# Kernel tuning notes

Measured on AMD Instinct MI355X. Metric: run time of the kernel, lower is better.

The kernel has to match this reference:

```python
import jax, jax.numpy as jnp
import numpy as np

D_MODEL = 1024
N_HEAD = 16
HEAD_DIM = D_MODEL // N_HEAD
ROPE_BASE = 10000.0


def _weight_quant(w):
    # BitNet b1.58 ternary weight quant with per-tensor absmean scale (STE).
    scale = jnp.clip(jnp.mean(jnp.abs(w)), 1e-5, None)
    wq = jnp.clip(jnp.round(w / scale), -1.0, 1.0) * scale
    return w + jax.lax.stop_gradient(wq - w)


def _act_quant(x):
    # Per-token int8 absmax activation quant (STE).
    scale = 127.0 / jnp.clip(jnp.max(jnp.abs(x), axis=-1, keepdims=True), 1e-5, None)
    xq = jnp.clip(jnp.round(x * scale), -128.0, 127.0) / scale
    return x + jax.lax.stop_gradient(xq - x)


def _bitlinear(x, w):
    # y = act_quant(x) @ weight_quant(w).T   (torch Linear convention, no bias)
    return _act_quant(x) @ _weight_quant(w).T


def _rope(x, pos):
    # x: [B, H, T, D]; half-split rotation.
    d = x.shape[-1]
    inv_freq = 1.0 / (ROPE_BASE ** (jnp.arange(0, d, 2, dtype=jnp.float32) / d))
    ang = pos[:, None].astype(jnp.float32) * inv_freq[None, :]  # [T, D/2]
    cos, sin = jnp.cos(ang), jnp.sin(ang)
    x1, x2 = x[..., : d // 2], x[..., d // 2 :]
    return jnp.concatenate([x1 * cos - x2 * sin, x1 * sin + x2 * cos], axis=-1)


def setup_inputs() -> dict:
    key = jax.random.key(0)
    k0, k1, k2, k3, k4 = jax.random.split(key, 5)
    B, T = 2, 2048
    s = 1.0 / np.sqrt(D_MODEL)
    return {
        "x": jax.random.normal(k0, (B, T, D_MODEL), dtype=jnp.float32),
        "Wq": jax.random.normal(k1, (D_MODEL, D_MODEL), dtype=jnp.float32) * s,
        "Wk": jax.random.normal(k2, (D_MODEL, D_MODEL), dtype=jnp.float32) * s,
        "Wv": jax.random.normal(k3, (D_MODEL, D_MODEL), dtype=jnp.float32) * s,
        "Wo": jax.random.normal(k4, (D_MODEL, D_MODEL), dtype=jnp.float32) * s,
    }


def reference(x, Wq, Wk, Wv, Wo):
    B, T, C = x.shape
    pos = jnp.arange(T)
    def heads(y):
        return y.reshape(B, T, N_HEAD, HEAD_DIM).transpose(0, 2, 1, 3)  # [B,H,T,D]
    q = _rope(heads(_bitlinear(x, Wq)), pos)
    k = _rope(heads(_bitlinear(x, Wk)), pos)
    v = heads(_bitlinear(x, Wv))
    scores = jnp.einsum("bhqd,bhkd->bhqk", q, k) / jnp.sqrt(jnp.float32(HEAD_DIM))
    causal = jnp.tril(jnp.ones((T, T), dtype=bool))
    scores = jnp.where(causal[None, None], scores, jnp.finfo(scores.dtype).min)
    att = jax.nn.softmax(scores, axis=-1)
    y = jnp.einsum("bhqk,bhkd->bhqd", att, v)  # [B,H,T,D]
    y = y.transpose(0, 2, 1, 3).reshape(B, T, C)
    return _bitlinear(y, Wo)
```

## Files before the change

### kernel.cpp

```cpp
#include <hip/hip_runtime.h>
#include <hip/hip_bf16.h>
#include <math.h>

typedef __bf16 bf16_t;
typedef signed char i8_t;
typedef __attribute__((ext_vector_type(8))) __bf16 bf16x8;
typedef __attribute__((ext_vector_type(4))) __bf16 bf16x4;
typedef __attribute__((ext_vector_type(4))) float f32x4;
typedef __attribute__((ext_vector_type(4))) int i32x4;

typedef __attribute__((address_space(3))) void lds_void_t;
typedef const __attribute__((address_space(1))) void glb_void_t;
#define GLOAD_LDS(g, l) __builtin_amdgcn_global_load_lds((glb_void_t*)(g), (lds_void_t*)(l), 16, 0, 0)

#define MFMA16(a,b,c) __builtin_amdgcn_mfma_f32_16x16x32_bf16(a,b,c,0,0,0)
#define MFMAI8(a,b,c) __builtin_amdgcn_mfma_i32_16x16x64_i8(a,b,c,0,0,0)

#if __has_builtin(__builtin_amdgcn_exp2f)
#define EXP2F(x) __builtin_amdgcn_exp2f(x)
#else
#define EXP2F(x) exp2f(x)
#endif

static constexpr int TSEQ = 2048;
static constexpr int CDIM = 1024;
#define NEG_BIG (-1.0e30f)
#define Q_PRESCALE 0.18033688011112042f
#define ROPE_C 0.41524101190971284f

__global__ __launch_bounds__(256) void wreduce(const float* __restrict__ W0, const float* __restrict__ W1,
                                               const float* __restrict__ W2, const float* __restrict__ W3,
                                               double* __restrict__ partial) {
  int w = blockIdx.x >> 6, b = blockIdx.x & 63;
  const float* W = (w==0)?W0:(w==1)?W1:(w==2)?W2:W3;
  const float* base = W + (size_t)b * 16384;
  double s = 0.0;
  for (int i = threadIdx.x * 4; i < 16384; i += 1024) {
    float4 v = *(const float4*)(base + i);
    s += (double)fabsf(v.x) + (double)fabsf(v.y) + (double)fabsf(v.z) + (double)fabsf(v.w);
  }
  #pragma unroll
  for (int off = 1; off < 64; off <<= 1) s += __shfl_xor(s, off);
  __shared__ double red[4];
  if ((threadIdx.x & 63) == 0) red[threadIdx.x >> 6] = s;
  __syncthreads();
  if (threadIdx.x == 0) partial[blockIdx.x] = red[0] + red[1] + red[2] + red[3];
}

__global__ __launch_bounds__(256) void prep(const float* __restrict__ W0, const float* __restrict__ W1,
                                            const float* __restrict__ W2, const float* __restrict__ W3,
                                            const double* __restrict__ partial, float* __restrict__ wscale,
                                            i8_t* __restrict__ wq_all,
                                            const float* __restrict__ xg, i8_t* __restrict__ xqg,
                                            float* __restrict__ rowfac, float2* __restrict__ ropetab) {
  int bid = blockIdx.x;
  if (bid < 4096) {
    int w = bid >> 10;
    double ssum = 0.0;
    for (int i = 0; i < 64; ++i) ssum += partial[w * 64 + i];
    float s = fmaxf((float)(ssum * (1.0 / 1048576.0)), 1e-5f);
    if ((bid & 1023) == 0 && threadIdx.x == 0) wscale[w] = s;
    const float* W = (w==0)?W0:(w==1)?W1:(w==2)?W2:W3;
    int off = ((bid & 1023) * 256 + threadIdx.x) * 4;
    float4 v = *(const float4*)(W + off);
    char4 q;
    q.x = (i8_t)(int)fminf(fmaxf(rintf(v.x / s), -1.f), 1.f);
    q.y = (i8_t)(int)fminf(fmaxf(rintf(v.y / s), -1.f), 1.f);
    q.z = (i8_t)(int)fminf(fmaxf(rintf(v.z / s), -1.f), 1.f);
    q.w = (i8_t)(int)fminf(fmaxf(rintf(v.w / s), -1.f), 1.f);
    *(char4*)(wq_all + (size_t)w * 1048576 + off) = q;
  } else if (bid < 8192) {
    int r = bid - 4096;
    float4 v = *(const float4*)(xg + (size_t)r * 1024 + threadIdx.x * 4);
    float mx = fmaxf(fmaxf(fabsf(v.x), fabsf(v.y)), fmaxf(fabsf(v.z), fabsf(v.w)));
    #pragma unroll
    for (int off = 1; off < 64; off <<= 1) mx = fmaxf(mx, __shfl_xor(mx, off));
    __shared__ float red[4];
    if ((threadIdx.x & 63) == 0) red[threadIdx.x >> 6] = mx;
    __syncthreads();
    mx = fmaxf(fmaxf(red[0], red[1]), fmaxf(red[2], red[3]));
    mx = fmaxf(mx, 1e-5f);
    float scale = 127.0f / mx;
    if (threadIdx.x == 0) rowfac[r] = mx * (1.0f / 127.0f);
    char4 q;
    q.x = (i8_t)(int)fminf(fmaxf(rintf(v.x * scale), -128.f), 127.f);
    q.y = (i8_t)(int)fminf(fmaxf(rintf(v.y * scale), -128.f), 127.f);
    q.z = (i8_t)(int)fminf(fmaxf(rintf(v.z * scale), -128.f), 127.f);
    q.w = (i8_t)(int)fminf(fmaxf(rintf(v.w * scale), -128.f), 127.f);
    *(char4*)(xqg + (size_t)r * 1024 + threadIdx.x * 4) = q;
  } else {
    int t = (bid - 8192) * 8 + (threadIdx.x >> 5);
    int ii = threadIdx.x & 31;
    float ang = (float)t * exp2f(-(float)ii * ROPE_C);
    float sn, cs;
    sincosf(ang, &sn, &cs);
    ropetab[t * 32 + ii] = make_float2(cs, sn);
  }
}

__global__ __launch_bounds__(256) void actquant(const float* __restrict__ xg, i8_t* __restrict__ xqg,
                                                float* __restrict__ rowfac) {
  int r = blockIdx.x;
  float4 v = *(const float4*)(xg + (size_t)r * 1024 + threadIdx.x * 4);
  float mx = fmaxf(fmaxf(fabsf(v.x), fabsf(v.y)), fmaxf(fabsf(v.z), fabsf(v.w)));
  #pragma unroll
  for (int off = 1; off < 64; off <<= 1) mx = fmaxf(mx, __shfl_xor(mx, off));
  __shared__ float red[4];
  if ((threadIdx.x & 63) == 0) red[threadIdx.x >> 6] = mx;
  __syncthreads();
  mx = fmaxf(fmaxf(red[0], red[1]), fmaxf(red[2], red[3]));
  mx = fmaxf(mx, 1e-5f);
  float scale = 127.0f / mx;
  if (threadIdx.x == 0) rowfac[r] = mx * (1.0f / 127.0f);
  char4 q;
  q.x = (i8_t)(int)fminf(fmaxf(rintf(v.x * scale), -128.f), 127.f);
  q.y = (i8_t)(int)fminf(fmaxf(rintf(v.y * scale), -128.f), 127.f);
  q.z = (i8_t)(int)fminf(fmaxf(rintf(v.z * scale), -128.f), 127.f);
  q.w = (i8_t)(int)fminf(fmaxf(rintf(v.w * scale), -128.f), 127.f);
  *(char4*)(xqg + (size_t)r * 1024 + threadIdx.x * 4) = q;
}

__global__ __launch_bounds__(256) void gemm_qkv(const i8_t* __restrict__ xq, const i8_t* __restrict__ wq_all,
                                                const float* __restrict__ wscale, const float* __restrict__ rowfac,
                                                const float2* __restrict__ ropetab,
                                                bf16_t* __restrict__ qb, bf16_t* __restrict__ kb,
                                                bf16_t* __restrict__ vtb) {
  const int z = blockIdx.z;
  const i8_t* Bw = wq_all + (size_t)z * 1048576;
  const int m0 = blockIdx.x * 128, n0 = blockIdx.y * 128;
  const int tid = threadIdx.x;
  const int wave = tid >> 6, lane = tid & 63, quad = lane >> 4, l16 = lane & 15;
  const int wm = wave >> 1, wn = wave & 1;
  __shared__ __align__(16) i8_t As[128 * 64];
  __shared__ __align__(16) i8_t Bs[128 * 64];
  i32x4 zero = {0, 0, 0, 0};
  i32x4 acc[4][4];
  #pragma unroll
  for (int i = 0; i < 4; ++i)
    #pragma unroll
    for (int j = 0; j < 4; ++j) acc[i][j] = zero;

  const int row_s = tid >> 2;
  const int cg16 = (((tid & 3) - (row_s >> 1)) & 3) * 16;
  const int sw16 = ((quad + (l16 >> 1)) & 3) * 16;

  for (int kt = 0; kt < 16; ++kt) {
    __syncthreads();
    #pragma unroll
    for (int v2 = 0; v2 < 2; ++v2) {
      int v = tid + v2 * 256;
      int row = row_s + v2 * 64;
      GLOAD_LDS(&xq[(size_t)(m0 + row) * 1024 + kt * 64 + cg16], &As[v * 16]);
      GLOAD_LDS(&Bw[(size_t)(n0 + row) * 1024 + kt * 64 + cg16], &Bs[v * 16]);
    }
    __syncthreads();
    i32x4 af[4], bfr[4];
    #pragma unroll
    for (int i = 0; i < 4; ++i) af[i] = *(const i32x4*)&As[(wm * 64 + i * 16 + l16) * 64 + sw16];
    #pragma unroll
    for (int j = 0; j < 4; ++j) bfr[j] = *(const i32x4*)&Bs[(wn * 64 + j * 16 + l16) * 64 + sw16];
    if (z == 2) {
      #pragma unroll
      for (int i = 0; i < 4; ++i)
        #pragma unroll
        for (int j = 0; j < 4; ++j) acc[i][j] = MFMAI8(bfr[i], af[j], acc[i][j]);
    } else {
      #pragma unroll
      for (int i = 0; i < 4; ++i)
        #pragma unroll
        for (int j = 0; j < 4; ++j) acc[i][j] = MFMAI8(af[i], bfr[j], acc[i][j]);
    }
  }
  float ws = wscale[z] * (z == 0 ? Q_PRESCALE : 1.0f);
  if (z <= 1) {
    bf16_t* dst = (z == 0) ? qb : kb;
    const int h = (n0 >> 6) + wn;
    #pragma unroll
    for (int i = 0; i < 4; ++i) {
      #pragma unroll
      for (int r = 0; r < 4; ++r) {
        int m = m0 + wm * 64 + i * 16 + quad * 4 + r;
        float rf = rowfac[m] * ws;
        int b = m >> 11, t = m & 2047;
        bf16_t* drow = dst + (((size_t)b * 16 + h) * 2048 + t) * 64;
        #pragma unroll
        for (int j = 0; j < 2; ++j) {
          int dd1 = j * 16 + l16;
          float2 cs2 = ropetab[t * 32 + dd1];
          float v1 = (float)acc[i][j][r] * rf;
          float v2 = (float)acc[i][j + 2][r] * rf;
          drow[dd1]      = (bf16_t)(v1 * cs2.x - v2 * cs2.y);
          drow[dd1 + 32] = (bf16_t)(v1 * cs2.y + v2 * cs2.x);
        }
      }
    }
  } else {
    const int b = m0 >> 11;
    const int tbase = (m0 & 2047) + wm * 64;
    float rfj[4];
    #pragma unroll
    for (int j = 0; j < 4; ++j) rfj[j] = rowfac[m0 + wm * 64 + j * 16 + l16] * ws;
    #pragma unroll
    for (int i = 0; i < 4; ++i) {
      #pragma unroll
      for (int r = 0; r < 4; ++r) {
        int nrow = n0 + wn * 64 + i * 16 + quad * 4 + r;
        int h = nrow >> 6, dd = nrow & 63;
        bf16_t* vrow = vtb + (((size_t)b * 16 + h) * 64 + dd) * 2048 + tbase;
        #pragma unroll
        for (int j = 0; j < 4; ++j) vrow[j * 16 + l16] = (bf16_t)((float)acc[i][j][r] * rfj[j]);
      }
    }
  }
}

__global__ __launch_bounds__(256) void gemm_out(const i8_t* __restrict__ yq, const i8_t* __restrict__ wo,
                                                const float* __restrict__ wscale, const float* __restrict__ rowfac,
                                                float* __restrict__ out) {
  const int m0 = blockIdx.x * 128, n0 = blockIdx.y * 128;
  const int tid = threadIdx.x;
  const int wave = tid >> 6, lane = tid & 63, quad = lane >> 4, l16 = lane & 15;
  const int wm = wave >> 1, wn = wave & 1;
  __shared__ __align__(16) i8_t As[128 * 64];
  __shared__ __align__(16) i8_t Bs[128 * 64];
  i32x4 zero = {0, 0, 0, 0};
  i32x4 acc[4][4];
  #pragma unroll
  for (int i = 0; i < 4; ++i)
    #pragma unroll
    for (int j = 0; j < 4; ++j) acc[i][j] = zero;

  const int row_s = tid >> 2;
  const int cg16 = (((tid & 3) - (row_s >> 1)) & 3) * 16;
  const int sw16 = ((quad + (l16 >> 1)) & 3) * 16;

  for (int kt = 0; kt < 16; ++kt) {
    __syncthreads();
    #pragma unroll
    for (int v2 = 0; v2 < 2; ++v2) {
      int v = tid + v2 * 256;
      int row = row_s + v2 * 64;
      GLOAD_LDS(&yq[(size_t)(m0 + row) * 1024 + kt * 64 + cg16], &As[v * 16]);
      GLOAD_LDS(&wo[(size_t)(n0 + row) * 1024 + kt * 64 + cg16], &Bs[v * 16]);
    }
    __syncthreads();
    i32x4 af[4], bfr[4];
    #pragma unroll
    for (int i = 0; i < 4; ++i) af[i] = *(const i32x4*)&As[(wm * 64 + i * 16 + l16) * 64 + sw16];
    #pragma unroll
    for (int j = 0; j < 4; ++j) bfr[j] = *(const i32x4*)&Bs[(wn * 64 + j * 16 + l16) * 64 + sw16];
    #pragma unroll
    for (int i = 0; i < 4; ++i)
      #pragma unroll
      for (int j = 0; j < 4; ++j) acc[i][j] = MFMAI8(af[i], bfr[j], acc[i][j]);
  }
  float ws = wscale[3];
  #pragma unroll
  for (int i = 0; i < 4; ++i) {
    #pragma unroll
    for (int r = 0; r < 4; ++r) {
      int m = m0 + wm * 64 + i * 16 + quad * 4 + r;
      float rf = rowfac[m] * ws;
      #pragma unroll
      for (int j = 0; j < 4; ++j) {
        int n = n0 + wn * 64 + j * 16 + l16;
        out[(size_t)m * 1024 + n] = (float)acc[i][j][r] * rf;
      }
    }
  }
}

__global__ __launch_bounds__(256) void flash_attn(const bf16_t* __restrict__ qg, const bf16_t* __restrict__ kg,
                                                  const bf16_t* __restrict__ vtg, float* __restrict__ yf) {
  const int lid = (int)blockIdx.y * 8 + (int)blockIdx.x;
  const int p  = (lid >> 3) & 15;
  const int bh = (lid & 7) * 4 + (lid >> 7);
  const int tid = threadIdx.x;
  const int wave = tid >> 6, lane = tid & 63;
  const int quad = lane >> 4, l16 = lane & 15;

  __shared__ __align__(16) bf16_t Kb[2][64 * 64];
  __shared__ __align__(16) bf16_t Vb[2][64 * 64];
  __shared__ __align__(16) bf16_t Pl[4][16 * 72];

  const int b = bh >> 4, h = bh & 15;
  bf16_t* Pw = &Pl[wave][0];

  const int r0 = tid >> 3, cblk = tid & 7;
  const int swz8 = ((cblk ^ (r0 & 7)) * 8);
  const int ldsOffA = r0 * 64 + swz8;
  const int ldsOffB = ldsOffA + 32 * 64;
  const size_t bhbase = (size_t)bh * 131072;
  const bf16_t* kbaseA = kg + bhbase + r0 * 64 + cblk * 8;
  const bf16_t* kbaseB = kbaseA + 32 * 64;
  const bf16_t* vbaseA = vtg + bhbase + r0 * 2048 + cblk * 8;
  const bf16_t* vbaseB = vbaseA + 32 * 2048;

  int kf_off[4][2];
  #pragma unroll
  for (int n = 0; n < 4; ++n)
    #pragma unroll
    for (int c = 0; c < 2; ++c)
      kf_off[n][c] = (n * 16 + l16) * 64 + (((c * 4 + quad) ^ (l16 & 7)) * 8);

  bf16x8 ones;
  #pragma unroll
  for (int j = 0; j < 8; ++j) ones[j] = (bf16_t)1.0f;
  f32x4 zero = {0.f, 0.f, 0.f, 0.f};

  bf16x8 kpreA = *(const bf16x8*)(kbaseA);
  bf16x8 kpreB = *(const bf16x8*)(kbaseB);
  bf16x8 vpreA = *(const bf16x8*)(vbaseA);
  bf16x8 vpreB = *(const bf16x8*)(vbaseB);

  int cum = 0;
  #pragma unroll 1
  for (int tsel = 0; tsel < 2; ++tsel) {
    const int qt = tsel ? (31 - p) : p;
    const int kcmax = qt;
    const int qbw = qt * 64 + wave * 16;

    const bf16_t* qrowp = qg + ((size_t)bh * TSEQ + qbw + l16) * 64;
    bf16x8 aq0 = *(const bf16x8*)(qrowp + quad * 8);
    bf16x8 aq1 = *(const bf16x8*)(qrowp + 32 + quad * 8);

    f32x4 o[4], o5;
    #pragma unroll
    for (int i = 0; i < 4; ++i) o[i] = zero;
    o5 = zero;

    #pragma unroll 1
    for (int kc = 0; kc <= kcmax; ++kc, ++cum) {
      const int buf = cum & 1;
      bf16_t* Kt = &Kb[buf][0];
      bf16_t* Vt = &Vb[buf][0];
      *(bf16x8*)&Kt[ldsOffA] = kpreA;
      *(bf16x8*)&Kt[ldsOffB] = kpreB;
      *(bf16x8*)&Vt[ldsOffA] = vpreA;
      *(bf16x8*)&Vt[ldsOffB] = vpreB;
      __syncthreads();
      int nkc = (kc < kcmax) ? (kc + 1) : ((tsel == 0) ? 0 : -1);
      if (nkc >= 0) {
        kpreA = *(const bf16x8*)(kbaseA + nkc * 4096);
        kpreB = *(const bf16x8*)(kbaseB + nkc * 4096);
        vpreA = *(const bf16x8*)(vbaseA + nkc * 64);
        vpreB = *(const bf16x8*)(vbaseB + nkc * 64);
      }

      f32x4 s[4];
      #pragma unroll
      for (int n = 0; n < 4; ++n) {
        bf16x8 bk0 = *(const bf16x8*)&Kt[kf_off[n][0]];
        bf16x8 bk1 = *(const bf16x8*)&Kt[kf_off[n][1]];
        s[n] = MFMA16(aq1, bk1, MFMA16(aq0, bk0, zero));
      }
      if (kc * 64 + 63 > qbw) {
        #pragma unroll
        for (int n = 0; n < 4; ++n)
          #pragma unroll
          for (int r = 0; r < 4; ++r) {
            int kpos = kc * 64 + n * 16 + l16;
            int qpos = qbw + quad * 4 + r;
            if (kpos > qpos) s[n][r] = NEG_BIG;
          }
      }
      #pragma unroll
      for (int n = 0; n < 4; ++n)
        #pragma unroll
        for (int r = 0; r < 4; ++r)
          Pw[(quad * 4 + r) * 72 + n * 16 + l16] = (bf16_t)EXP2F(s[n][r]);

      bf16x8 ap0 = *(const bf16x8*)&Pw[l16 * 72 + quad * 8];
      bf16x8 ap1 = *(const bf16x8*)&Pw[l16 * 72 + 32 + quad * 8];
      #pragma unroll
      for (int nh = 0; nh < 4; ++nh) {
        bf16x8 bv0 = *(const bf16x8*)&Vt[kf_off[nh][0]];
        bf16x8 bv1 = *(const bf16x8*)&Vt[kf_off[nh][1]];
        o[nh] = MFMA16(ap1, bv1, MFMA16(ap0, bv0, o[nh]));
      }
      o5 = MFMA16(ap1, ones, MFMA16(ap0, ones, o5));
    }

    #pragma unroll
    for (int r = 0; r < 4; ++r) {
      float invl = 1.0f / o5[r];
      int t = qbw + quad * 4 + r;
      float* yrow = yf + ((size_t)b * TSEQ + t) * CDIM + h * 64;
      #pragma unroll
      for (int nh = 0; nh < 4; ++nh) yrow[nh * 16 + l16] = o[nh][r] * invl;
    }
  }
}

extern "C" void kernel_launch(void* const* d_in, const int* in_sizes, int n_in,
                              void* d_out, int out_size, void* d_ws, size_t ws_size,
                              hipStream_t stream) {
  const float* x  = (const float*)d_in[0];
  const float* Wq = (const float*)d_in[1];
  const float* Wk = (const float*)d_in[2];
  const float* Wv = (const float*)d_in[3];
  const float* Wo = (const float*)d_in[4];
  float* out = (float*)d_out;

  char* ws = (char*)d_ws;
  double* wpartial = (double*)(ws);
  float* wscale   = (float*)(ws + 4096);
  float* rowfacx  = (float*)(ws + 8192);
  float* rowfacy  = (float*)(ws + 8192 + 16384);
  i8_t* wq_all    = (i8_t*)(ws + 65536);
  i8_t* xq        = wq_all + 4194304;
  bf16_t* qb      = (bf16_t*)(xq + 4194304);
  bf16_t* kb      = qb + 4194304;
  bf16_t* vtb     = kb + 4194304;
  float*  yf      = (float*)(vtb + 4194304);
  float2* ropetab = (float2*)(yf + 4194304);
  i8_t* yq        = xq;

  wreduce<<<256, 256, 0, stream>>>(Wq, Wk, Wv, Wo, wpartial);
  prep<<<8448, 256, 0, stream>>>(Wq, Wk, Wv, Wo, wpartial, wscale, wq_all, x, xq, rowfacx, ropetab);
  gemm_qkv<<<dim3(32, 8, 3), 256, 0, stream>>>(xq, wq_all, wscale, rowfacx, ropetab, qb, kb, vtb);
  flash_attn<<<dim3(8, 64), 256, 0, stream>>>(qb, kb, vtb, yf);
  actquant<<<4096, 256, 0, stream>>>(yf, yq, rowfacy);
  gemm_out<<<dim3(32, 8), 256, 0, stream>>>(yq, wq_all + 3 * 1048576, wscale, rowfacy, out);
}
```

Before: 181.8 us.

## Give each attention block one 128-row query tile with 32 rows per wave

Result: no change. 180.5 us (-0.7%).

```diff
diff --git a/kernel.cpp b/kernel.cpp
--- a/kernel.cpp
+++ b/kernel.cpp
@@ -273,15 +273,16 @@
 __global__ __launch_bounds__(256) void flash_attn(const bf16_t* __restrict__ qg, const bf16_t* __restrict__ kg,
                                                   const bf16_t* __restrict__ vtg, float* __restrict__ yf) {
   const int lid = (int)blockIdx.y * 8 + (int)blockIdx.x;
-  const int p  = (lid >> 3) & 15;
-  const int bh = (lid & 7) * 4 + (lid >> 7);
+  const int p   = (lid >> 3) & 7;
+  const int bh  = (lid & 7) * 4 + ((lid >> 6) & 3);
+  const int qt  = (lid >> 8) ? (15 - p) : p;
   const int tid = threadIdx.x;
   const int wave = tid >> 6, lane = tid & 63;
   const int quad = lane >> 4, l16 = lane & 15;
 
   __shared__ __align__(16) bf16_t Kb[2][64 * 64];
   __shared__ __align__(16) bf16_t Vb[2][64 * 64];
-  __shared__ __align__(16) bf16_t Pl[4][16 * 72];
+  __shared__ __align__(16) bf16_t Pl[4][32 * 72];
 
   const int b = bh >> 4, h = bh & 15;
   bf16_t* Pw = &Pl[wave][0];
@@ -308,88 +309,113 @@
   for (int j = 0; j < 8; ++j) ones[j] = (bf16_t)1.0f;
   f32x4 zero = {0.f, 0.f, 0.f, 0.f};
 
+  const int kcmax = 2 * qt + 1;
+  const int qb0 = qt * 128 + wave * 32;
+
+  bf16x8 aq[2][2];
+  #pragma unroll
+  for (int i = 0; i < 2; ++i) {
+    const bf16_t* qrowp = qg + ((size_t)bh * TSEQ + qb0 + i * 16 + l16) * 64;
+    aq[i][0] = *(const bf16x8*)(qrowp + quad * 8);
+    aq[i][1] = *(const bf16x8*)(qrowp + 32 + quad * 8);
+  }
+
+  f32x4 o[2][4], o5[2];
+  #pragma unroll
+  for (int i = 0; i < 2; ++i) {
+    #pragma unroll
+    for (int n = 0; n < 4; ++n) o[i][n] = zero;
+    o5[i] = zero;
+  }
+
   bf16x8 kpreA = *(const bf16x8*)(kbaseA);
   bf16x8 kpreB = *(const bf16x8*)(kbaseB);
   bf16x8 vpreA = *(const bf16x8*)(vbaseA);
   bf16x8 vpreB = *(const bf16x8*)(vbaseB);
 
-  int cum = 0;
   #pragma unroll 1
-  for (int tsel = 0; tsel < 2; ++tsel) {
-    const int qt = tsel ? (31 - p) : p;
-    const int kcmax = qt;
-    const int qbw = qt * 64 + wave * 16;
-
-    const bf16_t* qrowp = qg + ((size_t)bh * TSEQ + qbw + l16) * 64;
-    bf16x8 aq0 = *(const bf16x8*)(qrowp + quad * 8);
-    bf16x8 aq1 = *(const bf16x8*)(qrowp + 32 + quad * 8);
-
-    f32x4 o[4], o5;
-    #pragma unroll
-    for (int i = 0; i < 4; ++i) o[i] = zero;
-    o5 = zero;
-
-    #pragma unroll 1
-    for (int kc = 0; kc <= kcmax; ++kc, ++cum) {
-      const int buf = cum & 1;
-      bf16_t* Kt = &Kb[buf][0];
-      bf16_t* Vt = &Vb[buf][0];
-      *(bf16x8*)&Kt[ldsOffA] = kpreA;
-      *(bf16x8*)&Kt[ldsOffB] = kpreB;
-      *(bf16x8*)&Vt[ldsOffA] = vpreA;
-      *(bf16x8*)&Vt[ldsOffB] = vpreB;
-      __syncthreads();
-      int nkc = (kc < kcmax) ? (kc + 1) : ((tsel == 0) ? 0 : -1);
-      if (nkc >= 0) {
-        kpreA = *(const bf16x8*)(kbaseA + nkc * 4096);
-        kpreB = *(const bf16x8*)(kbaseB + nkc * 4096);
-        vpreA = *(const bf16x8*)(vbaseA + nkc * 64);
-        vpreB = *(const bf16x8*)(vbaseB + nkc * 64);
-      }
-
-      f32x4 s[4];
-      #pragma unroll
-      for (int n = 0; n < 4; ++n) {
-        bf16x8 bk0 = *(const bf16x8*)&Kt[kf_off[n][0]];
-        bf16x8 bk1 = *(const bf16x8*)&Kt[kf_off[n][1]];
-        s[n] = MFMA16(aq1, bk1, MFMA16(aq0, bk0, zero));
-      }
-      if (kc * 64 + 63 > qbw) {
+  for (int kc = 0; kc <= kcmax; ++kc) {
+    const int buf = kc & 1;
+    bf16_t* Kt = &Kb[buf][0];
+    bf16_t* Vt = &Vb[buf][0];
+    *(bf16x8*)&Kt[ldsOffA] = kpreA;
+    *(bf16x8*)&Kt[ldsOffB] = kpreB;
+    *(bf16x8*)&Vt[ldsOffA] = vpreA;
+    *(bf16x8*)&Vt[ldsOffB] = vpreB;
+    __syncthreads();
+    if (kc < kcmax) {
+      kpreA = *(const bf16x8*)(kbaseA + (kc + 1) * 4096);
+      kpreB = *(const bf16x8*)(kbaseB + (kc + 1) * 4096);
+      vpreA = *(const bf16x8*)(vbaseA + (kc + 1) * 64);
+      vpreB = *(const bf16x8*)(vbaseB + (kc + 1) * 64);
+    }
+
+    if (kc * 64 > qb0 + 31) continue;
+
+    bf16x8 bk[4][2];
+    #pragma unroll
+    for (int n = 0; n < 4; ++n) {
+      bk[n][0] = *(const bf16x8*)&Kt[kf_off[n][0]];
+      bk[n][1] = *(const bf16x8*)&Kt[kf_off[n][1]];
+    }
+    f32x4 s[2][4];
+    __builtin_amdgcn_s_setprio(1);
+    #pragma unroll
+    for (int i = 0; i < 2; ++i)
+      #pragma unroll
+      for (int n = 0; n < 4; ++n)
+        s[i][n] = MFMA16(aq[i][1], bk[n][1], MFMA16(aq[i][0], bk[n][0], zero));
+    __builtin_amdgcn_s_setprio(0);
+
+    if (kc * 64 + 63 > qb0) {
+      #pragma unroll
+      for (int i = 0; i < 2; ++i)
         #pragma unroll
         for (int n = 0; n < 4; ++n)
           #pragma unroll
           for (int r = 0; r < 4; ++r) {
             int kpos = kc * 64 + n * 16 + l16;
-            int qpos = qbw + quad * 4 + r;
-            if (kpos > qpos) s[n][r] = NEG_BIG;
+            int qpos = qb0 + i * 16 + quad * 4 + r;
+            if (kpos > qpos) s[i][n][r] = NEG_BIG;
           }
-      }
+    }
+    #pragma unroll
+    for (int i = 0; i < 2; ++i)
       #pragma unroll
       for (int n = 0; n < 4; ++n)
         #pragma unroll
         for (int r = 0; r < 4; ++r)
-          Pw[(quad * 4 + r) * 72 + n * 16 + l16] = (bf16_t)EXP2F(s[n][r]);
-
-      bf16x8 ap0 = *(const bf16x8*)&Pw[l16 * 72 + quad * 8];
-      bf16x8 ap1 = *(const bf16x8*)&Pw[l16 * 72 + 32 + quad * 8];
-      #pragma unroll
-      for (int nh = 0; nh < 4; ++nh) {
-        bf16x8 bv0 = *(const bf16x8*)&Vt[kf_off[nh][0]];
-        bf16x8 bv1 = *(const bf16x8*)&Vt[kf_off[nh][1]];
-        o[nh] = MFMA16(ap1, bv1, MFMA16(ap0, bv0, o[nh]));
-      }
-      o5 = MFMA16(ap1, ones, MFMA16(ap0, ones, o5));
-    }
-
+          Pw[(i * 16 + quad * 4 + r) * 72 + n * 16 + l16] = (bf16_t)EXP2F(s[i][n][r]);
+
+    bf16x8 bv[4][2];
+    #pragma unroll
+    for (int nh = 0; nh < 4; ++nh) {
+      bv[nh][0] = *(const bf16x8*)&Vt[kf_off[nh][0]];
+      bv[nh][1] = *(const bf16x8*)&Vt[kf_off[nh][1]];
+    }
+    __builtin_amdgcn_s_setprio(1);
+    #pragma unroll
+    for (int i = 0; i < 2; ++i) {
+      bf16x8 ap0 = *(const bf16x8*)&Pw[(i * 16 + l16) * 72 + quad * 8];
+      bf16x8 ap1 = *(const bf16x8*)&Pw[(i * 16 + l16) * 72 + 32 + quad * 8];
+      #pragma unroll
+      for (int nh = 0; nh < 4; ++nh)
+        o[i][nh] = MFMA16(ap1, bv[nh][1], MFMA16(ap0, bv[nh][0], o[i][nh]));
+      o5[i] = MFMA16(ap1, ones, MFMA16(ap0, ones, o5[i]));
+    }
+    __builtin_amdgcn_s_setprio(0);
+  }
+
+  #pragma unroll
+  for (int i = 0; i < 2; ++i)
     #pragma unroll
     for (int r = 0; r < 4; ++r) {
-      float invl = 1.0f / o5[r];
-      int t = qbw + quad * 4 + r;
+      float invl = 1.0f / o5[i][r];
+      int t = qb0 + i * 16 + quad * 4 + r;
       float* yrow = yf + ((size_t)b * TSEQ + t) * CDIM + h * 64;
       #pragma unroll
-      for (int nh = 0; nh < 4; ++nh) yrow[nh * 16 + l16] = o[nh][r] * invl;
-    }
-  }
+      for (int nh = 0; nh < 4; ++nh) yrow[nh * 16 + l16] = o[i][nh][r] * invl;
+    }
 }
 
 extern "C" void kernel_launch(void* const* d_in, const int* in_sizes, int n_in,
```
